# Kernel optimization log

Hardware: AMD Instinct MI355X
Metric: run time of the kernel (lower is better)

Reference implementation:

```python
import jax, jax.numpy as jnp
from jax import lax
import numpy as np

T, N, IN_DIM, H = 128, 512, 512, 512
LN_EPS = 1e-5


def setup_inputs() -> dict:
    key = jax.random.key(0)
    ks = jax.random.split(key, 8)
    x = jax.random.normal(ks[0], (T * N, IN_DIM), dtype=jnp.float32)
    hxs = jax.random.normal(ks[1], (N, H), dtype=jnp.float32)
    masks = (jax.random.uniform(ks[2], (T * N, 1)) > 0.1).astype(jnp.float32)
    # GRU params (single layer), torch layout: weight_ih (3H, IN), weight_hh (3H, H)
    W_ih = jax.random.normal(ks[3], (3 * H, IN_DIM), dtype=jnp.float32) / np.sqrt(IN_DIM)
    W_hh = jax.random.normal(ks[4], (3 * H, H), dtype=jnp.float32) / np.sqrt(H)
    b_ih = jnp.zeros((3 * H,), dtype=jnp.float32)
    b_hh = jnp.zeros((3 * H,), dtype=jnp.float32)
    ln_w = jnp.ones((H,), dtype=jnp.float32)
    ln_b = jnp.zeros((H,), dtype=jnp.float32)
    return {"x": x, "hxs": hxs, "masks": masks, "W_ih": W_ih, "W_hh": W_hh,
            "b_ih": b_ih, "b_hh": b_hh, "ln_w": ln_w, "ln_b": ln_b}


def reference(x, hxs, masks, W_ih, W_hh, b_ih, b_hh, ln_w, ln_b):
    n_env, hid = hxs.shape
    t_steps = x.shape[0] // n_env
    xs = x.reshape(t_steps, n_env, -1)          # (T, N, IN)
    ms = masks.reshape(t_steps, n_env, 1)       # (T, N, 1)

    def step(h, inp):
        xt, mt = inp
        h = h * mt                               # reset hidden where mask == 0
        gi = xt @ W_ih.T + b_ih                  # (N, 3H)
        gh = h @ W_hh.T + b_hh                   # (N, 3H)
        i_r, i_z, i_n = jnp.split(gi, 3, axis=-1)
        h_r, h_z, h_n = jnp.split(gh, 3, axis=-1)
        r = jax.nn.sigmoid(i_r + h_r)
        z = jax.nn.sigmoid(i_z + h_z)
        n = jnp.tanh(i_n + r * h_n)
        h_new = (1.0 - z) * n + z * h            # torch GRU convention
        return h_new, h_new

    h_last, outs = lax.scan(step, hxs, (xs, ms))
    stacked = outs.reshape(t_steps * n_env, hid)
    mu = jnp.mean(stacked, axis=-1, keepdims=True)
    var = jnp.var(stacked, axis=-1, keepdims=True)
    normed = (stacked - mu) * lax.rsqrt(var + LN_EPS) * ln_w + ln_b
    return normed, h_last
```

## Files before the change

kernel.cpp:

```cpp
#include <hip/hip_runtime.h>


typedef __attribute__((ext_vector_type(8))) __bf16 bf16x8;
typedef __attribute__((ext_vector_type(4)))  float f32x4;
typedef __attribute__((ext_vector_type(16))) float f32x16;

__device__ __forceinline__ unsigned short f2bf(float f) {
  unsigned u = __builtin_bit_cast(unsigned, f);
  u += 0x7FFFu + ((u >> 16) & 1u);
  return (unsigned short)(u >> 16);
}
__device__ __forceinline__ float bf2f(unsigned short h) {
  unsigned u = ((unsigned)h) << 16;
  return __builtin_bit_cast(float, u);
}
__device__ __forceinline__ float sigm(float x) { return 1.0f / (1.0f + __expf(-x)); }
__device__ __forceinline__ float tanh_fast(float x) {
  float t = __expf(2.0f * x);
  return 1.0f - 2.0f / (t + 1.0f);
}

#define GI_BYTES   ((size_t)65536 * 1536 * 2)
#define WHH_OFF    GI_BYTES
#define WHH_BYTES  ((size_t)1536 * 512 * 2)
#define HB_OFF     (WHH_OFF + WHH_BYTES)
#define HB_BYTES   ((size_t)2 * 512 * 512 * 2)
#define CNT_OFF    (HB_OFF + HB_BYTES)

__global__ __launch_bounds__(256) void prep_kernel(const float* __restrict__ whh,
                                                   unsigned short* __restrict__ whh_bf,
                                                   unsigned int* __restrict__ cnt) {
  int i = blockIdx.x * 256 + threadIdx.x;
  for (int j = i; j < 1536 * 512; j += 1024 * 256) whh_bf[j] = f2bf(whh[j]);
  if (i < 2048) cnt[i] = 0u;
}

__global__ __launch_bounds__(256) void gi_gemm(const float* __restrict__ x,
                                               const float* __restrict__ wih,
                                               const float* __restrict__ bih,
                                               const float* __restrict__ bhh,
                                               unsigned short* __restrict__ gi) {
  __shared__ unsigned short As[128 * 72];
  __shared__ unsigned short Bs[128 * 72];
  const int tid = threadIdx.x;
  const int rb = blockIdx.x * 128;
  const int jb = blockIdx.y * 128;
  const int wave = tid >> 6, lane = tid & 63;
  const int wm = wave >> 1, wn = wave & 1;
  const int quad = lane >> 4, l16 = lane & 15;

  f32x4 acc[4][4];
  const f32x4 zero4 = {0.f, 0.f, 0.f, 0.f};
  for (int a = 0; a < 4; ++a)
    for (int b = 0; b < 4; ++b) acc[a][b] = zero4;

  for (int kb = 0; kb < 512; kb += 64) {
    __syncthreads();
#pragma unroll
    for (int j = 0; j < 8; ++j) {
      int f = tid * 4 + j * 1024;
      int r = f >> 6, k = f & 63;
      float4 av = *(const float4*)(x + (size_t)(rb + r) * 512 + kb + k);
      ushort4 a4;
      a4.x = f2bf(av.x); a4.y = f2bf(av.y); a4.z = f2bf(av.z); a4.w = f2bf(av.w);
      *(ushort4*)(As + r * 72 + k) = a4;
      float4 bv = *(const float4*)(wih + (size_t)(jb + r) * 512 + kb + k);
      ushort4 b4;
      b4.x = f2bf(bv.x); b4.y = f2bf(bv.y); b4.z = f2bf(bv.z); b4.w = f2bf(bv.w);
      *(ushort4*)(Bs + r * 72 + k) = b4;
    }
    __syncthreads();
#pragma unroll
    for (int kk = 0; kk < 64; kk += 32) {
      bf16x8 af[4], bfr[4];
#pragma unroll
      for (int mi = 0; mi < 4; ++mi)
        af[mi] = *(const bf16x8*)(As + (wm * 64 + mi * 16 + l16) * 72 + kk + quad * 8);
#pragma unroll
      for (int ni = 0; ni < 4; ++ni)
        bfr[ni] = *(const bf16x8*)(Bs + (wn * 64 + ni * 16 + l16) * 72 + kk + quad * 8);
#pragma unroll
      for (int mi = 0; mi < 4; ++mi)
#pragma unroll
        for (int ni = 0; ni < 4; ++ni)
          acc[mi][ni] = __builtin_amdgcn_mfma_f32_16x16x32_bf16(af[mi], bfr[ni],
                                                                acc[mi][ni], 0, 0, 0);
    }
  }
#pragma unroll
  for (int ni = 0; ni < 4; ++ni) {
    int jcol = jb + wn * 64 + ni * 16 + l16;
    float bias = bih[jcol] + (jcol < 1024 ? bhh[jcol] : 0.0f);
#pragma unroll
    for (int mi = 0; mi < 4; ++mi) {
#pragma unroll
      for (int reg = 0; reg < 4; ++reg) {
        int grow = rb + wm * 64 + mi * 16 + quad * 4 + reg;
        gi[(size_t)grow * 1536 + jcol] = f2bf(acc[mi][ni][reg] + bias);
      }
    }
  }
}

#define HL_STRIDE 520

__global__ __launch_bounds__(384, 2) void rec_kernel(
    const float* __restrict__ hxs, const float* __restrict__ masks,
    const float* __restrict__ bhh, const unsigned short* __restrict__ gi,
    const unsigned short* __restrict__ whh_bf,
    unsigned short* hb, unsigned int* cnt, float* __restrict__ out) {
  __shared__ unsigned short Hl[32 * HL_STRIDE];
  __shared__ float gatesL[3 * 32 * 64];

  const int tid = threadIdx.x;
  const int bid = blockIdx.x;
  const int g = bid >> 3;
  const int eb = g * 32;
  const int cb = (bid & 7) * 64;
  const int wave = tid >> 6;
  const int lane = tid & 63;
  const int l32 = lane & 31;
  const int lhi = lane >> 5;
  const int gate = wave >> 1;
  const int half = wave & 1;
  unsigned* hbu = (unsigned*)hb;

  bf16x8 wreg[32];
  {
    const unsigned short* wb =
        whh_bf + (((size_t)(gate * 512 + cb + half * 32 + l32)) << 9) + lhi * 8;
#pragma unroll
    for (int ks = 0; ks < 32; ++ks) wreg[ks] = *(const bf16x8*)(wb + (ks << 4));
  }

  float hr0[3], hr1[3];
  float bn0[3], bn1[3];
#pragma unroll
  for (int j = 0; j < 3; ++j) {
    int idx = tid + j * 384;
    if (idx < 1024) {
      int e = idx >> 5, cp = (idx & 31) << 1;
      float2 h2 = *(const float2*)(hxs + (size_t)(eb + e) * 512 + cb + cp);
      hr0[j] = h2.x; hr1[j] = h2.y;
      float2 bn2 = *(const float2*)(bhh + 1024 + cb + cp);
      bn0[j] = bn2.x; bn1[j] = bn2.y;
      unsigned pk = (unsigned)f2bf(h2.x) | ((unsigned)f2bf(h2.y) << 16);
      __hip_atomic_store(hbu + ((((unsigned)(eb + e) << 9) + cb + cp) >> 1), pk,
                         __ATOMIC_RELAXED, __HIP_MEMORY_SCOPE_AGENT);
    }
  }

  unsigned bt = 0;
  unsigned int* myflag = cnt + bid * 16;
  unsigned int* pollbase = cnt + (g * 8) * 16;

#define GROUP_BARRIER()                                                          \
  do {                                                                           \
    __syncthreads();                  \
    bt += 1;                                                                     \
    if (tid == 0)                                                                \
      __hip_atomic_store(myflag, bt, __ATOMIC_RELAXED, __HIP_MEMORY_SCOPE_AGENT);\
    if (tid < 64) {                                                              \
      unsigned int* fp = pollbase + (lane & 7) * 16;                             \
      int guard = 0;                                                             \
      for (;;) {                                                                 \
        unsigned v = __hip_atomic_load(fp, __ATOMIC_RELAXED,                     \
                                       __HIP_MEMORY_SCOPE_AGENT);                \
        if (__all(v >= bt)) break;                                               \
        __builtin_amdgcn_s_sleep(1);                                             \
        if (++guard > (1 << 20)) break;                                          \
      }                                                                          \
    }                                                                            \
    __syncthreads();                                                             \
  } while (0)

  GROUP_BARRIER();

  for (int t = 0; t < 128; ++t) {
    const unsigned hsrc = (unsigned)(t & 1) * 131072u;
    const unsigned hdst = (unsigned)((t & 1) ^ 1) * 131072u;

    for (int e = wave; e < 32; e += 6) {
      const unsigned* gp = hbu + hsrc + ((unsigned)(eb + e) << 8) + (lane << 2);
      __builtin_amdgcn_global_load_lds(
          (const __attribute__((address_space(1))) unsigned*)gp,
          (__attribute__((address_space(3))) unsigned*)(Hl + e * HL_STRIDE),
          16, 0, 17);
    }
    unsigned gr[3], gz[3], gn[3];
    float mk[3];
#pragma unroll
    for (int j = 0; j < 3; ++j) {
      int idx = tid + j * 384;
      if (idx < 1024) {
        int e = idx >> 5, cp = (idx & 31) << 1;
        const unsigned short* gp2 =
            gi + ((size_t)(t * 512 + eb + e) * 1536 + cb + cp);
        gr[j] = *(const unsigned*)gp2;
        gz[j] = *(const unsigned*)(gp2 + 512);
        gn[j] = *(const unsigned*)(gp2 + 1024);
        mk[j] = masks[t * 512 + eb + e];
      }
    }
    __syncthreads();

    f32x16 acc = {0.f, 0.f, 0.f, 0.f, 0.f, 0.f, 0.f, 0.f,
                  0.f, 0.f, 0.f, 0.f, 0.f, 0.f, 0.f, 0.f};
    const unsigned short* ap = Hl + l32 * HL_STRIDE + lhi * 8;
#pragma unroll
    for (int ks = 0; ks < 32; ++ks) {
      bf16x8 a = *(const bf16x8*)(ap + (ks << 4));
      acc = __builtin_amdgcn_mfma_f32_32x32x16_bf16(a, wreg[ks], acc, 0, 0, 0);
    }
    {
      float* gt = gatesL + gate * 2048 + half * 32;
#pragma unroll
      for (int reg = 0; reg < 16; ++reg) {
        int erow = (reg & 3) + 8 * (reg >> 2) + 4 * lhi;
        gt[erow * 64 + l32] = acc[reg];
      }
    }
    __syncthreads();

#pragma unroll
    for (int j = 0; j < 3; ++j) {
      int idx = tid + j * 384;
      if (idx < 1024) {
        int e = idx >> 5, cp = (idx & 31) << 1;
        float m = mk[j];
        int o = e * 64 + cp;
        float r0 = sigm(bf2f((unsigned short)gr[j]) + m * gatesL[o]);
        float r1 = sigm(bf2f((unsigned short)(gr[j] >> 16)) + m * gatesL[o + 1]);
        float z0 = sigm(bf2f((unsigned short)gz[j]) + m * gatesL[2048 + o]);
        float z1 = sigm(bf2f((unsigned short)(gz[j] >> 16)) + m * gatesL[2048 + o + 1]);
        float n0 = tanh_fast(bf2f((unsigned short)gn[j]) +
                             r0 * (m * gatesL[4096 + o] + bn0[j]));
        float n1 = tanh_fast(bf2f((unsigned short)(gn[j] >> 16)) +
                             r1 * (m * gatesL[4096 + o + 1] + bn1[j]));
        float h0 = hr0[j] * m;
        float h1 = hr1[j] * m;
        float hn0 = (1.0f - z0) * n0 + z0 * h0;
        float hn1 = (1.0f - z1) * n1 + z1 * h1;
        hr0[j] = hn0; hr1[j] = hn1;
        float2 ov; ov.x = hn0; ov.y = hn1;
        *(float2*)(out + ((size_t)(t * 512 + eb + e)) * 512 + cb + cp) = ov;
        unsigned pk = (unsigned)f2bf(hn0) | ((unsigned)f2bf(hn1) << 16);
        __hip_atomic_store(hbu + hdst + ((((unsigned)(eb + e) << 9) + cb + cp) >> 1),
                           pk, __ATOMIC_RELAXED, __HIP_MEMORY_SCOPE_AGENT);
        if (t == 127) {
          *(float2*)(out + (size_t)33554432 + (size_t)(eb + e) * 512 + cb + cp) = ov;
        }
      }
    }
    GROUP_BARRIER();
  }
#undef GROUP_BARRIER
}

__global__ __launch_bounds__(256) void ln_kernel(float* __restrict__ out,
                                                 const float* __restrict__ lnw,
                                                 const float* __restrict__ lnb) {
  int row = blockIdx.x * 4 + (threadIdx.x >> 6);
  int lane = threadIdx.x & 63;
  float* p = out + (size_t)row * 512 + lane * 8;
  float4 v0 = *(float4*)p;
  float4 v1 = *(float4*)(p + 4);
  float s = v0.x + v0.y + v0.z + v0.w + v1.x + v1.y + v1.z + v1.w;
  float q = v0.x * v0.x + v0.y * v0.y + v0.z * v0.z + v0.w * v0.w +
            v1.x * v1.x + v1.y * v1.y + v1.z * v1.z + v1.w * v1.w;
#pragma unroll
  for (int m = 1; m < 64; m <<= 1) {
    s += __shfl_xor(s, m, 64);
    q += __shfl_xor(q, m, 64);
  }
  float mean = s * (1.0f / 512.0f);
  float var = q * (1.0f / 512.0f) - mean * mean;
  float rstd = rsqrtf(fmaxf(var, 0.0f) + 1e-5f);
  float4 w0 = *(const float4*)(lnw + lane * 8);
  float4 w1 = *(const float4*)(lnw + lane * 8 + 4);
  float4 b0 = *(const float4*)(lnb + lane * 8);
  float4 b1 = *(const float4*)(lnb + lane * 8 + 4);
  v0.x = (v0.x - mean) * rstd * w0.x + b0.x;
  v0.y = (v0.y - mean) * rstd * w0.y + b0.y;
  v0.z = (v0.z - mean) * rstd * w0.z + b0.z;
  v0.w = (v0.w - mean) * rstd * w0.w + b0.w;
  v1.x = (v1.x - mean) * rstd * w1.x + b1.x;
  v1.y = (v1.y - mean) * rstd * w1.y + b1.y;
  v1.z = (v1.z - mean) * rstd * w1.z + b1.z;
  v1.w = (v1.w - mean) * rstd * w1.w + b1.w;
  *(float4*)p = v0;
  *(float4*)(p + 4) = v1;
}

extern "C" void kernel_launch(void* const* d_in, const int* in_sizes, int n_in,
                              void* d_out, int out_size, void* d_ws, size_t ws_size,
                              hipStream_t stream) {
  const float* x    = (const float*)d_in[0];
  const float* hxs  = (const float*)d_in[1];
  const float* masks= (const float*)d_in[2];
  const float* wih  = (const float*)d_in[3];
  const float* whh  = (const float*)d_in[4];
  const float* bih  = (const float*)d_in[5];
  const float* bhh  = (const float*)d_in[6];
  const float* lnw  = (const float*)d_in[7];
  const float* lnb  = (const float*)d_in[8];
  float* out = (float*)d_out;
  char* ws = (char*)d_ws;

  unsigned short* gi     = (unsigned short*)ws;
  unsigned short* whh_bf = (unsigned short*)(ws + WHH_OFF);
  unsigned short* hb     = (unsigned short*)(ws + HB_OFF);
  unsigned int*   cnt    = (unsigned int*)(ws + CNT_OFF);

  prep_kernel<<<1024, 256, 0, stream>>>(whh, whh_bf, cnt);
  gi_gemm<<<dim3(512, 12), 256, 0, stream>>>(x, wih, bih, bhh, gi);
  rec_kernel<<<128, 384, 0, stream>>>(hxs, masks, bhh, gi, whh_bf, hb, cnt, out);
  ln_kernel<<<16384, 256, 0, stream>>>(out, lnw, lnb);
}
```

Baseline: 1.139 ms.

## Pre-convert inputs to bf16 for gi GEMM and software-pipeline recurrence steps

```diff
diff --git a/kernel.cpp b/kernel.cpp
--- a/kernel.cpp
+++ b/kernel.cpp
@@ -20,26 +20,118 @@
   return 1.0f - 2.0f / (t + 1.0f);
 }
 
-#define GI_BYTES   ((size_t)65536 * 1536 * 2)
-#define WHH_OFF    GI_BYTES
-#define WHH_BYTES  ((size_t)1536 * 512 * 2)
-#define HB_OFF     (WHH_OFF + WHH_BYTES)
-#define HB_BYTES   ((size_t)2 * 512 * 512 * 2)
-#define CNT_OFF    (HB_OFF + HB_BYTES)
+#define GI_BYTES    ((size_t)65536 * 1536 * 2)
+#define WHH_OFF     GI_BYTES
+#define WHH_BYTES   ((size_t)1536 * 512 * 2)
+#define HB_OFF      (WHH_OFF + WHH_BYTES)
+#define HB_BYTES    ((size_t)2 * 512 * 512 * 2)
+#define CNT_OFF     (HB_OFF + HB_BYTES)
+#define CNT_BYTES   ((size_t)8192)
+#define XBF_OFF     (CNT_OFF + CNT_BYTES)
+#define XBF_BYTES   ((size_t)32768 * 512 * 2)
+#define WIHBF_OFF   (XBF_OFF + XBF_BYTES)
+#define WIHBF_BYTES ((size_t)1536 * 512 * 2)
+#define WS_FAST     (WIHBF_OFF + WIHBF_BYTES)
 
 __global__ __launch_bounds__(256) void prep_kernel(const float* __restrict__ whh,
+                                                   const float* __restrict__ wih,
                                                    unsigned short* __restrict__ whh_bf,
-                                                   unsigned int* __restrict__ cnt) {
+                                                   unsigned short* __restrict__ wih_bf,
+                                                   unsigned int* __restrict__ cnt,
+                                                   int fast) {
   int i = blockIdx.x * 256 + threadIdx.x;
-  for (int j = i; j < 1536 * 512; j += 1024 * 256) whh_bf[j] = f2bf(whh[j]);
+  for (int j = i; j < 1536 * 512; j += 1024 * 256) {
+    whh_bf[j] = f2bf(whh[j]);
+    if (fast) wih_bf[j] = f2bf(wih[j]);
+  }
   if (i < 2048) cnt[i] = 0u;
 }
 
-__global__ __launch_bounds__(256) void gi_gemm(const float* __restrict__ x,
-                                               const float* __restrict__ wih,
-                                               const float* __restrict__ bih,
-                                               const float* __restrict__ bhh,
-                                               unsigned short* __restrict__ gi) {
+__global__ __launch_bounds__(256) void xconv_kernel(const float* __restrict__ xsrc,
+                                                    unsigned short* __restrict__ xbf) {
+  int i = blockIdx.x * 256 + threadIdx.x;
+  for (int j = i; j < 4194304; j += 1048576) {
+    float4 v = *((const float4*)xsrc + j);
+    ushort4 o;
+    o.x = f2bf(v.x); o.y = f2bf(v.y); o.z = f2bf(v.z); o.w = f2bf(v.w);
+    *((ushort4*)xbf + j) = o;
+  }
+}
+
+__global__ __launch_bounds__(256) void gi_gemm_bf16(const unsigned short* __restrict__ xbf,
+                                                    const unsigned short* __restrict__ wihbf,
+                                                    const float* __restrict__ bih,
+                                                    const float* __restrict__ bhh,
+                                                    unsigned short* __restrict__ gi,
+                                                    int r0) {
+  __shared__ unsigned short As[128 * 64];
+  __shared__ unsigned short Bs[128 * 64];
+  const int tid = threadIdx.x;
+  const int rb = blockIdx.x * 128;
+  const int jb = blockIdx.y * 128;
+  const int wave = tid >> 6, lane = tid & 63;
+  const int wm = wave >> 1, wn = wave & 1;
+  const int quad = lane >> 4, l16 = lane & 15;
+
+  f32x4 acc[4][4];
+  const f32x4 zero4 = {0.f, 0.f, 0.f, 0.f};
+  for (int a = 0; a < 4; ++a)
+    for (int b = 0; b < 4; ++b) acc[a][b] = zero4;
+
+  for (int kb = 0; kb < 512; kb += 64) {
+    __syncthreads();
+#pragma unroll
+    for (int r = 0; r < 4; ++r) {
+      const int fbase = (r * 256 + wave * 64) * 8;
+      const int f = fbase + lane * 8;
+      const int row = f >> 6, col = f & 63;
+      __builtin_amdgcn_global_load_lds(
+          (const __attribute__((address_space(1))) unsigned*)
+              (xbf + (size_t)(rb + row) * 512 + kb + col),
+          (__attribute__((address_space(3))) unsigned*)(As + fbase), 16, 0, 0);
+      __builtin_amdgcn_global_load_lds(
+          (const __attribute__((address_space(1))) unsigned*)
+              (wihbf + (size_t)(jb + row) * 512 + kb + col),
+          (__attribute__((address_space(3))) unsigned*)(Bs + fbase), 16, 0, 0);
+    }
+    __syncthreads();
+#pragma unroll
+    for (int kk = 0; kk < 64; kk += 32) {
+      bf16x8 af[4], bfr[4];
+#pragma unroll
+      for (int mi = 0; mi < 4; ++mi)
+        af[mi] = *(const bf16x8*)(As + (wm * 64 + mi * 16 + l16) * 64 + kk + quad * 8);
+#pragma unroll
+      for (int ni = 0; ni < 4; ++ni)
+        bfr[ni] = *(const bf16x8*)(Bs + (wn * 64 + ni * 16 + l16) * 64 + kk + quad * 8);
+#pragma unroll
+      for (int mi = 0; mi < 4; ++mi)
+#pragma unroll
+        for (int ni = 0; ni < 4; ++ni)
+          acc[mi][ni] = __builtin_amdgcn_mfma_f32_16x16x32_bf16(af[mi], bfr[ni],
+                                                                acc[mi][ni], 0, 0, 0);
+    }
+  }
+#pragma unroll
+  for (int ni = 0; ni < 4; ++ni) {
+    int jcol = jb + wn * 64 + ni * 16 + l16;
+    float bias = bih[jcol] + (jcol < 1024 ? bhh[jcol] : 0.0f);
+#pragma unroll
+    for (int mi = 0; mi < 4; ++mi) {
+#pragma unroll
+      for (int reg = 0; reg < 4; ++reg) {
+        int grow = r0 + rb + wm * 64 + mi * 16 + quad * 4 + reg;
+        gi[(size_t)grow * 1536 + jcol] = f2bf(acc[mi][ni][reg] + bias);
+      }
+    }
+  }
+}
+
+__global__ __launch_bounds__(256) void gi_gemm_f32(const float* __restrict__ x,
+                                                   const float* __restrict__ wih,
+                                                   const float* __restrict__ bih,
+                                                   const float* __restrict__ bhh,
+                                                   unsigned short* __restrict__ gi) {
   __shared__ unsigned short As[128 * 72];
   __shared__ unsigned short Bs[128 * 72];
   const int tid = threadIdx.x;
@@ -104,7 +196,108 @@
 
 #define HL_STRIDE 520
 
-__global__ __launch_bounds__(384, 2) void rec_kernel(
+#define REC_STEP(T, HSRC, HDST, GRc, GZc, GNc, MKc, GRn, GZn, GNn, MKn)        \
+  {                                                                            \
+    for (int e = wave; e < 32; e += 6) {                                       \
+      const unsigned* gp = hbu + (HSRC) + ((unsigned)(eb + e) << 8) + (lane << 2); \
+      __builtin_amdgcn_global_load_lds(                                        \
+          (const __attribute__((address_space(1))) unsigned*)gp,               \
+          (__attribute__((address_space(3))) unsigned*)(Hl + e * HL_STRIDE),   \
+          16, 0, 17);                                                          \
+    }                                                                          \
+    __syncthreads();                   \
+    if ((T) < 127) {                                                           \
+      _Pragma("unroll")                                                        \
+      for (int j = 0; j < 3; ++j) {                                            \
+        int idx = tid + j * 384;                                               \
+        if (idx < 1024) {                                                      \
+          int e = idx >> 5, cp = (idx & 31) << 1;                              \
+          const unsigned short* gp2 =                                          \
+              gi + ((size_t)(((T) + 1) * 512 + eb + e) * 1536 + cb + cp);      \
+          GRn[j] = *(const unsigned*)gp2;                                      \
+          GZn[j] = *(const unsigned*)(gp2 + 512);                              \
+          GNn[j] = *(const unsigned*)(gp2 + 1024);                             \
+          MKn[j] = masks[((T) + 1) * 512 + eb + e];                            \
+        }                                                                      \
+      }                                                                        \
+    }                                                                          \
+                  \
+    f32x16 acc0 = zeroacc, acc1 = zeroacc;                                     \
+    {                                                                          \
+      const unsigned short* ap = Hl + l32 * HL_STRIDE + lhi * 8;               \
+      _Pragma("unroll")                                                        \
+      for (int ks = 0; ks < 32; ks += 2) {                                     \
+        bf16x8 a0 = *(const bf16x8*)(ap + (ks << 4));                          \
+        bf16x8 a1 = *(const bf16x8*)(ap + ((ks + 1) << 4));                    \
+        acc0 = __builtin_amdgcn_mfma_f32_32x32x16_bf16(a0, wreg[ks], acc0, 0, 0, 0); \
+        acc1 = __builtin_amdgcn_mfma_f32_32x32x16_bf16(a1, wreg[ks + 1], acc1, 0, 0, 0); \
+      }                                                                        \
+    }                                                                          \
+    {                                                                          \
+      float* gt = gatesL + gate * 2048 + half * 32;                            \
+      _Pragma("unroll")                                                        \
+      for (int reg = 0; reg < 16; ++reg) {                                     \
+        int erow = (reg & 3) + 8 * (reg >> 2) + 4 * lhi;                       \
+        gt[erow * 64 + l32] = acc0[reg] + acc1[reg];                           \
+      }                                                                        \
+    }                                                                          \
+    __syncthreads();                                     \
+    _Pragma("unroll")                                                          \
+    for (int j = 0; j < 3; ++j) {                                              \
+      int idx = tid + j * 384;                                                 \
+      if (idx < 1024) {                                                        \
+        int e = idx >> 5, cp = (idx & 31) << 1;                                \
+        float m = MKc[j];                                                      \
+        int o = e * 64 + cp;                                                   \
+        float r0 = sigm(bf2f((unsigned short)GRc[j]) + m * gatesL[o]);         \
+        float r1 = sigm(bf2f((unsigned short)(GRc[j] >> 16)) + m * gatesL[o + 1]); \
+        float z0 = sigm(bf2f((unsigned short)GZc[j]) + m * gatesL[2048 + o]);  \
+        float z1 = sigm(bf2f((unsigned short)(GZc[j] >> 16)) + m * gatesL[2048 + o + 1]); \
+        float n0 = tanh_fast(bf2f((unsigned short)GNc[j]) +                    \
+                             r0 * (m * gatesL[4096 + o] + bn0[j]));            \
+        float n1 = tanh_fast(bf2f((unsigned short)(GNc[j] >> 16)) +            \
+                             r1 * (m * gatesL[4096 + o + 1] + bn1[j]));        \
+        float h0 = hr0[j] * m;                                                 \
+        float h1 = hr1[j] * m;                                                 \
+        float hn0 = (1.0f - z0) * n0 + z0 * h0;                                \
+        float hn1 = (1.0f - z1) * n1 + z1 * h1;                                \
+        hr0[j] = hn0; hr1[j] = hn1;                                            \
+        unsigned pk = (unsigned)f2bf(hn0) | ((unsigned)f2bf(hn1) << 16);       \
+        __hip_atomic_store(hbu + (HDST) + ((((unsigned)(eb + e) << 9) + cb + cp) >> 1), \
+                           pk, __ATOMIC_RELAXED, __HIP_MEMORY_SCOPE_AGENT);    \
+      }                                                                        \
+    }                                                                          \
+    __syncthreads();          \
+    bt += 1;                                                                   \
+    if (tid == 0)                                                              \
+      __hip_atomic_store(myflag, bt, __ATOMIC_RELAXED, __HIP_MEMORY_SCOPE_AGENT); \
+         \
+    _Pragma("unroll")                                                          \
+    for (int j = 0; j < 3; ++j) {                                              \
+      int idx = tid + j * 384;                                                 \
+      if (idx < 1024) {                                                        \
+        int e = idx >> 5, cp = (idx & 31) << 1;                                \
+        float2 ov; ov.x = hr0[j]; ov.y = hr1[j];                               \
+        *(float2*)(out + ((size_t)((T) * 512 + eb + e)) * 512 + cb + cp) = ov; \
+        if ((T) == 127)                                                        \
+          *(float2*)(out + (size_t)33554432 + (size_t)(eb + e) * 512 + cb + cp) = ov; \
+      }                                                                        \
+    }                                                                          \
+    if (tid < 64) {                                                            \
+      unsigned int* fp = pollbase + (lane & 7) * 16;                           \
+      int guard = 0;                                                           \
+      for (;;) {                                                               \
+        unsigned v = __hip_atomic_load(fp, __ATOMIC_RELAXED,                   \
+                                       __HIP_MEMORY_SCOPE_AGENT);              \
+        if (__all(v >= bt)) break;                                             \
+        __builtin_amdgcn_s_sleep(1);                                           \
+        if (++guard > (1 << 20)) break;                                        \
+      }                                                                        \
+    }                                                                          \
+    __syncthreads();                                          \
+  }
+
+__global__ __launch_bounds__(384, 1) void rec_kernel(
     const float* __restrict__ hxs, const float* __restrict__ masks,
     const float* __restrict__ bhh, const unsigned short* __restrict__ gi,
     const unsigned short* __restrict__ whh_bf,
@@ -125,6 +318,9 @@
   const int half = wave & 1;
   unsigned* hbu = (unsigned*)hb;
 
+  const f32x16 zeroacc = {0.f, 0.f, 0.f, 0.f, 0.f, 0.f, 0.f, 0.f,
+                          0.f, 0.f, 0.f, 0.f, 0.f, 0.f, 0.f, 0.f};
+
   bf16x8 wreg[32];
   {
     const unsigned short* wb =
@@ -154,108 +350,46 @@
   unsigned int* myflag = cnt + bid * 16;
   unsigned int* pollbase = cnt + (g * 8) * 16;
 
-#define GROUP_BARRIER()                                                          \
-  do {                                                                           \
-    __syncthreads();                  \
-    bt += 1;                                                                     \
-    if (tid == 0)                                                                \
-      __hip_atomic_store(myflag, bt, __ATOMIC_RELAXED, __HIP_MEMORY_SCOPE_AGENT);\
-    if (tid < 64) {                                                              \
-      unsigned int* fp = pollbase + (lane & 7) * 16;                             \
-      int guard = 0;                                                             \
-      for (;;) {                                                                 \
-        unsigned v = __hip_atomic_load(fp, __ATOMIC_RELAXED,                     \
-                                       __HIP_MEMORY_SCOPE_AGENT);                \
-        if (__all(v >= bt)) break;                                               \
-        __builtin_amdgcn_s_sleep(1);                                             \
-        if (++guard > (1 << 20)) break;                                          \
-      }                                                                          \
-    }                                                                            \
-    __syncthreads();                                                             \
-  } while (0)
-
-  GROUP_BARRIER();
-
-  for (int t = 0; t < 128; ++t) {
-    const unsigned hsrc = (unsigned)(t & 1) * 131072u;
-    const unsigned hdst = (unsigned)((t & 1) ^ 1) * 131072u;
-
-    for (int e = wave; e < 32; e += 6) {
-      const unsigned* gp = hbu + hsrc + ((unsigned)(eb + e) << 8) + (lane << 2);
-      __builtin_amdgcn_global_load_lds(
-          (const __attribute__((address_space(1))) unsigned*)gp,
-          (__attribute__((address_space(3))) unsigned*)(Hl + e * HL_STRIDE),
-          16, 0, 17);
-    }
-    unsigned gr[3], gz[3], gn[3];
-    float mk[3];
-#pragma unroll
-    for (int j = 0; j < 3; ++j) {
-      int idx = tid + j * 384;
-      if (idx < 1024) {
-        int e = idx >> 5, cp = (idx & 31) << 1;
-        const unsigned short* gp2 =
-            gi + ((size_t)(t * 512 + eb + e) * 1536 + cb + cp);
-        gr[j] = *(const unsigned*)gp2;
-        gz[j] = *(const unsigned*)(gp2 + 512);
-        gn[j] = *(const unsigned*)(gp2 + 1024);
-        mk[j] = masks[t * 512 + eb + e];
-      }
-    }
-    __syncthreads();
-
-    f32x16 acc = {0.f, 0.f, 0.f, 0.f, 0.f, 0.f, 0.f, 0.f,
-                  0.f, 0.f, 0.f, 0.f, 0.f, 0.f, 0.f, 0.f};
-    const unsigned short* ap = Hl + l32 * HL_STRIDE + lhi * 8;
-#pragma unroll
-    for (int ks = 0; ks < 32; ++ks) {
-      bf16x8 a = *(const bf16x8*)(ap + (ks << 4));
-      acc = __builtin_amdgcn_mfma_f32_32x32x16_bf16(a, wreg[ks], acc, 0, 0, 0);
-    }
-    {
-      float* gt = gatesL + gate * 2048 + half * 32;
-#pragma unroll
-      for (int reg = 0; reg < 16; ++reg) {
-        int erow = (reg & 3) + 8 * (reg >> 2) + 4 * lhi;
-        gt[erow * 64 + l32] = acc[reg];
-      }
-    }
-    __syncthreads();
-
-#pragma unroll
-    for (int j = 0; j < 3; ++j) {
-      int idx = tid + j * 384;
-      if (idx < 1024) {
-        int e = idx >> 5, cp = (idx & 31) << 1;
-        float m = mk[j];
-        int o = e * 64 + cp;
-        float r0 = sigm(bf2f((unsigned short)gr[j]) + m * gatesL[o]);
-        float r1 = sigm(bf2f((unsigned short)(gr[j] >> 16)) + m * gatesL[o + 1]);
-        float z0 = sigm(bf2f((unsigned short)gz[j]) + m * gatesL[2048 + o]);
-        float z1 = sigm(bf2f((unsigned short)(gz[j] >> 16)) + m * gatesL[2048 + o + 1]);
-        float n0 = tanh_fast(bf2f((unsigned short)gn[j]) +
-                             r0 * (m * gatesL[4096 + o] + bn0[j]));
-        float n1 = tanh_fast(bf2f((unsigned short)(gn[j] >> 16)) +
-                             r1 * (m * gatesL[4096 + o + 1] + bn1[j]));
-        float h0 = hr0[j] * m;
-        float h1 = hr1[j] * m;
-        float hn0 = (1.0f - z0) * n0 + z0 * h0;
-        float hn1 = (1.0f - z1) * n1 + z1 * h1;
-        hr0[j] = hn0; hr1[j] = hn1;
-        float2 ov; ov.x = hn0; ov.y = hn1;
-        *(float2*)(out + ((size_t)(t * 512 + eb + e)) * 512 + cb + cp) = ov;
-        unsigned pk = (unsigned)f2bf(hn0) | ((unsigned)f2bf(hn1) << 16);
-        __hip_atomic_store(hbu + hdst + ((((unsigned)(eb + e) << 9) + cb + cp) >> 1),
-                           pk, __ATOMIC_RELAXED, __HIP_MEMORY_SCOPE_AGENT);
-        if (t == 127) {
-          *(float2*)(out + (size_t)33554432 + (size_t)(eb + e) * 512 + cb + cp) = ov;
-        }
-      }
-    }
-    GROUP_BARRIER();
-  }
-#undef GROUP_BARRIER
-}
+  unsigned grA[3], gzA[3], gnA[3];
+  unsigned grB[3], gzB[3], gnB[3];
+  float mkA[3], mkB[3];
+#pragma unroll
+  for (int j = 0; j < 3; ++j) {
+    int idx = tid + j * 384;
+    if (idx < 1024) {
+      int e = idx >> 5, cp = (idx & 31) << 1;
+      const unsigned short* gp2 = gi + ((size_t)(eb + e) * 1536 + cb + cp);
+      grA[j] = *(const unsigned*)gp2;
+      gzA[j] = *(const unsigned*)(gp2 + 512);
+      gnA[j] = *(const unsigned*)(gp2 + 1024);
+      mkA[j] = masks[eb + e];
+    }
+  }
+
+  __syncthreads();
+  bt += 1;
+  if (tid == 0)
+    __hip_atomic_store(myflag, bt, __ATOMIC_RELAXED, __HIP_MEMORY_SCOPE_AGENT);
+  if (tid < 64) {
+    unsigned int* fp = pollbase + (lane & 7) * 16;
+    int guard = 0;
+    for (;;) {
+      unsigned v = __hip_atomic_load(fp, __ATOMIC_RELAXED, __HIP_MEMORY_SCOPE_AGENT);
+      if (__all(v >= bt)) break;
+      __builtin_amdgcn_s_sleep(1);
+      if (++guard > (1 << 20)) break;
+    }
+  }
+  __syncthreads();
+
+  for (int u = 0; u < 64; ++u) {
+    const int te = 2 * u;
+    const int to = 2 * u + 1;
+    REC_STEP(te, 0u, 131072u, grA, gzA, gnA, mkA, grB, gzB, gnB, mkB);
+    REC_STEP(to, 131072u, 0u, grB, gzB, gnB, mkB, grA, gzA, gnA, mkA);
+  }
+}
+#undef REC_STEP
 
 __global__ __launch_bounds__(256) void ln_kernel(float* __restrict__ out,
                                                  const float* __restrict__ lnw,
@@ -311,9 +445,19 @@
   unsigned short* whh_bf = (unsigned short*)(ws + WHH_OFF);
   unsigned short* hb     = (unsigned short*)(ws + HB_OFF);
   unsigned int*   cnt    = (unsigned int*)(ws + CNT_OFF);
-
-  prep_kernel<<<1024, 256, 0, stream>>>(whh, whh_bf, cnt);
-  gi_gemm<<<dim3(512, 12), 256, 0, stream>>>(x, wih, bih, bhh, gi);
+  unsigned short* xbf    = (unsigned short*)(ws + XBF_OFF);
+  unsigned short* wih_bf = (unsigned short*)(ws + WIHBF_OFF);
+  const int fast = (ws_size >= WS_FAST) ? 1 : 0;
+
+  prep_kernel<<<1024, 256, 0, stream>>>(whh, wih, whh_bf, wih_bf, cnt, fast);
+  if (fast) {
+    xconv_kernel<<<4096, 256, 0, stream>>>(x, xbf);
+    gi_gemm_bf16<<<dim3(256, 12), 256, 0, stream>>>(xbf, wih_bf, bih, bhh, gi, 0);
+    xconv_kernel<<<4096, 256, 0, stream>>>(x + (size_t)32768 * 512, xbf);
+    gi_gemm_bf16<<<dim3(256, 12), 256, 0, stream>>>(xbf, wih_bf, bih, bhh, gi, 32768);
+  } else {
+    gi_gemm_f32<<<dim3(512, 12), 256, 0, stream>>>(x, wih, bih, bhh, gi);
+  }
   rec_kernel<<<128, 384, 0, stream>>>(hxs, masks, bhh, gi, whh_bf, hb, cnt, out);
   ln_kernel<<<16384, 256, 0, stream>>>(out, lnw, lnb);
 }
```

After: 993.6 us. 12.8% less time.
